# Performance work log

Hardware: AMD Instinct MI355X
Metric: run time of the kernel (lower is better)

## Reference

```python
import jax, jax.numpy as jnp
import numpy as np


def setup_inputs() -> dict:
    key = jax.random.key(0)
    k1, k2 = jax.random.split(key)
    B, S, D = 4, 2048, 1024
    x = jax.random.normal(k1, (B, S, D), dtype=jnp.float32)
    # uniform initializer in keras is small; scale to keep softmax well-behaved
    kernel = jax.random.normal(k2, (3, D, D), dtype=jnp.float32) * 0.02
    return {"x": x, "kernel": kernel}


def reference(x, kernel):
    # x: [B, S, D], kernel: [3, D, D]
    D = x.shape[-1]
    q = jnp.einsum('bsd,de->bse', x, kernel[0])
    k = jnp.einsum('bsd,de->bse', x, kernel[1])
    v = jnp.einsum('bsd,de->bse', x, kernel[2])
    scores = jnp.einsum('bqe,bke->bqk', q, k) / jnp.sqrt(jnp.float32(D))
    attn = jax.nn.softmax(scores, axis=-1)
    return jnp.einsum('bqk,bke->bqe', attn, v)
```

## Files before the change

### kernel.cpp

```cpp
#include <hip/hip_runtime.h>
#include <hip/hip_cooperative_groups.h>
#include <hip/hip_bf16.h>
#include <cstdint>

namespace cg = cooperative_groups;

typedef __bf16 bf16x8 __attribute__((ext_vector_type(8)));
typedef float f32x4 __attribute__((ext_vector_type(4)));

struct SharedMem {
  unsigned short As[2][4096];
  unsigned short Bs[2][4096];
};

__device__ __forceinline__ unsigned short f2bf(float f) {
  union { float f; uint32_t u; } a; a.f = f;
  uint32_t r = a.u + 0x7fffu + ((a.u >> 16) & 1u);
  return (unsigned short)(r >> 16);
}
__device__ __forceinline__ void gload_lds16(const unsigned short* g, unsigned short* l) {
  __builtin_amdgcn_global_load_lds(
      (const __attribute__((address_space(1))) void*)g,
      (__attribute__((address_space(3))) void*)l, 16, 0, 0);
}

template <int NJ>
__device__ __forceinline__ void gemm_tile_core(
    const unsigned short* __restrict__ A, const unsigned short* __restrict__ Bt,
    int K, SharedMem& sh, f32x4 (&acc)[4][NJ]) {
  const int t = threadIdx.x;
  const int lane = t & 63;
  const int quad = lane >> 4;
  const int l15 = lane & 15;
  const int wave = t >> 6;
  const int wm = (wave >> 1) * 64;
  const int wn = (wave & 1) * (NJ * 16);

  const int srow = t >> 2;
  const int scol = (((t & 3) ^ ((srow >> 1) & 3)) * 8);
  const unsigned short* ga = A + (size_t)srow * K + scol;
  const unsigned short* gb = Bt + (size_t)srow * K + scol;
  const size_t rowskip = (size_t)64 * K;

  const int swz = (quad ^ ((l15 >> 1) & 3)) * 8;
  const int aOff = (wm + l15) * 32 + swz;
  const int bOff = (wn + l15) * 32 + swz;

#pragma unroll
  for (int i = 0; i < 4; i++)
#pragma unroll
    for (int j = 0; j < NJ; j++) acc[i][j] = (f32x4){0.f, 0.f, 0.f, 0.f};

  gload_lds16(ga, &sh.As[0][t * 8]);
  gload_lds16(ga + rowskip, &sh.As[0][2048 + t * 8]);
  gload_lds16(gb, &sh.Bs[0][t * 8]);
  if (NJ == 4) gload_lds16(gb + rowskip, &sh.Bs[0][2048 + t * 8]);

  int buf = 0;
  for (int k0 = 0; k0 < K; k0 += 32, buf ^= 1) {
    __syncthreads();
    if (k0 + 32 < K) {
      const int kn = k0 + 32;
      gload_lds16(ga + kn, &sh.As[buf ^ 1][t * 8]);
      gload_lds16(ga + rowskip + kn, &sh.As[buf ^ 1][2048 + t * 8]);
      gload_lds16(gb + kn, &sh.Bs[buf ^ 1][t * 8]);
      if (NJ == 4) gload_lds16(gb + rowskip + kn, &sh.Bs[buf ^ 1][2048 + t * 8]);
    }
    const unsigned short* aB = &sh.As[buf][aOff];
    const unsigned short* bB = &sh.Bs[buf][bOff];
    bf16x8 a[4], b[NJ];
#pragma unroll
    for (int i = 0; i < 4; i++) a[i] = *(const bf16x8*)(aB + i * 512);
#pragma unroll
    for (int j = 0; j < NJ; j++) b[j] = *(const bf16x8*)(bB + j * 512);
#pragma unroll
    for (int i = 0; i < 4; i++)
#pragma unroll
      for (int j = 0; j < NJ; j++)
        acc[i][j] = __builtin_amdgcn_mfma_f32_16x16x32_bf16(a[i], b[j], acc[i][j], 0, 0, 0);
  }
}


__device__ __forceinline__ void phase0_casts(const float* __restrict__ x,
                                             const float* __restrict__ W,
                                             unsigned short* __restrict__ xb,
                                             unsigned short* __restrict__ Wt,
                                             SharedMem& sh) {
  const int bid = blockIdx.x, t = threadIdx.x;
#pragma unroll
  for (int i = 0; i < 4; i++) {
    size_t idx = (((size_t)(bid + i * 1024)) * 256 + t) * 8;
    float4 a = *(const float4*)(x + idx);
    float4 b = *(const float4*)(x + idx + 4);
    uint4 o;
    o.x = (uint32_t)f2bf(a.x) | ((uint32_t)f2bf(a.y) << 16);
    o.y = (uint32_t)f2bf(a.z) | ((uint32_t)f2bf(a.w) << 16);
    o.z = (uint32_t)f2bf(b.x) | ((uint32_t)f2bf(b.y) << 16);
    o.w = (uint32_t)f2bf(b.z) | ((uint32_t)f2bf(b.w) << 16);
    *(uint4*)(xb + idx) = o;
  }
  float* tile = (float*)sh.As;
  const int tx = t & 31, ty = t >> 5;
  for (int i = 0; i < 3; i++) {
    const int u = bid + i * 1024;
    const int z = u >> 10, rest = u & 1023;
    const float* Wz = W + (size_t)z * 1048576;
    unsigned short* Wtz = Wt + (size_t)z * 1048576;
    const int x0 = (rest & 31) * 32, y0 = (rest >> 5) * 32;
#pragma unroll
    for (int ii = 0; ii < 32; ii += 8)
      tile[(ty + ii) * 33 + tx] = Wz[(size_t)(y0 + ty + ii) * 1024 + x0 + tx];
    __syncthreads();
#pragma unroll
    for (int ii = 0; ii < 32; ii += 8)
      Wtz[(size_t)(x0 + ty + ii) * 1024 + y0 + tx] = f2bf(tile[tx * 33 + ty + ii]);
    __syncthreads();
  }
}

__device__ __forceinline__ void phase1_qkv(const unsigned short* __restrict__ xb,
                                           const unsigned short* __restrict__ Wt,
                                           unsigned short* __restrict__ Q,
                                           unsigned short* __restrict__ Kb,
                                           unsigned short* __restrict__ Vt,
                                           SharedMem& sh) {
  const int t = threadIdx.x;
  const int lane = t & 63, quad = lane >> 4, l15 = lane & 15, wave = t >> 6;
  const int wm = (wave >> 1) * 64;
  for (int pass = 0; pass < 2; pass++) {
    const int v = blockIdx.x + pass * 1024;
    if (v >= 1536) break;
    const int z = v >> 9, mt = (v >> 3) & 63, nt = v & 7;
    const unsigned short* A = xb + (size_t)mt * 128 * 1024;
    const unsigned short* Bt = Wt + (size_t)z * 1048576 + (size_t)nt * 128 * 1024;
    f32x4 acc[4][4];
    gemm_tile_core<4>(A, Bt, 1024, sh, acc);
    const int mbase = mt * 128 + wm + quad * 4;
    const int nbase = nt * 128 + (wave & 1) * 64 + l15;
    if (z < 2) {
      unsigned short* C = (z == 0) ? Q : Kb;
#pragma unroll
      for (int mi = 0; mi < 4; mi++)
#pragma unroll
        for (int ni = 0; ni < 4; ni++) {
          const int m = mbase + mi * 16, n = nbase + ni * 16;
#pragma unroll
          for (int r = 0; r < 4; r++)
            C[(size_t)(m + r) * 1024 + n] = f2bf(acc[mi][ni][r]);
        }
    } else {
#pragma unroll
      for (int mi = 0; mi < 4; mi++) {
        const int m = mbase + mi * 16;
        const int b = m >> 11, s = m & 2047;
#pragma unroll
        for (int ni = 0; ni < 4; ni++) {
          const int n = nbase + ni * 16;
          uint2 val;
          val.x = (uint32_t)f2bf(acc[mi][ni][0]) | ((uint32_t)f2bf(acc[mi][ni][1]) << 16);
          val.y = (uint32_t)f2bf(acc[mi][ni][2]) | ((uint32_t)f2bf(acc[mi][ni][3]) << 16);
          *(uint2*)(Vt + (size_t)b * 2097152 + (size_t)n * 2048 + s) = val;
        }
      }
    }
  }
}

__device__ __forceinline__ void phase2_scores(const unsigned short* __restrict__ Q,
                                              const unsigned short* __restrict__ Kb,
                                              unsigned short* __restrict__ Sb,
                                              float* __restrict__ partial,
                                              SharedMem& sh) {
  const int t = threadIdx.x;
  const int lane = t & 63, quad = lane >> 4, l15 = lane & 15, wave = t >> 6;
  const int wm = (wave >> 1) * 64;
  const int v = blockIdx.x;
  const int z = v >> 8, mt = (v >> 4) & 15, nt = v & 15;
  const unsigned short* A = Q + (size_t)z * 2097152 + (size_t)mt * 128 * 1024;
  const unsigned short* Bt = Kb + (size_t)z * 2097152 + (size_t)nt * 128 * 1024;
  f32x4 acc[4][4];
  gemm_tile_core<4>(A, Bt, 1024, sh, acc);
  unsigned short* C = Sb + (size_t)z * 4194304;
  const int mbase = mt * 128 + wm + quad * 4;
  const int nbase = nt * 128 + (wave & 1) * 64 + l15;
  const int j = nt * 2 + (wave & 1);
#pragma unroll
  for (int mi = 0; mi < 4; mi++) {
#pragma unroll
    for (int r = 0; r < 4; r++) {
      const int m = mbase + mi * 16 + r;
      float s = 0.f;
#pragma unroll
      for (int ni = 0; ni < 4; ni++) {
        const float e = __expf(acc[mi][ni][r] * 0.03125f);
        C[(size_t)m * 2048 + nbase + ni * 16] = f2bf(e);
        s += e;
      }
      s += __shfl_xor(s, 1);
      s += __shfl_xor(s, 2);
      s += __shfl_xor(s, 4);
      s += __shfl_xor(s, 8);
      if (l15 == 0) partial[(size_t)j * 8192 + (size_t)z * 2048 + m] = s;
    }
  }
}

__device__ __forceinline__ void phase3_pv(const unsigned short* __restrict__ Sb,
                                          const unsigned short* __restrict__ Vt,
                                          const float* __restrict__ partial,
                                          float* __restrict__ out,
                                          SharedMem& sh) {
  const int t = threadIdx.x;
  const int lane = t & 63, quad = lane >> 4, l15 = lane & 15, wave = t >> 6;
  const int wm = (wave >> 1) * 64;
  const int v = blockIdx.x;
  const int z = v >> 8, mt = (v >> 4) & 15, et = v & 15;
  const unsigned short* A = Sb + (size_t)z * 4194304 + (size_t)mt * 128 * 2048;
  const unsigned short* Bt = Vt + (size_t)z * 2097152 + (size_t)et * 64 * 2048;
  f32x4 acc[4][2];
  gemm_tile_core<2>(A, Bt, 2048, sh, acc);
  __syncthreads();
  float* rowinv = (float*)sh.As;
  if (t < 128) {
    const size_t grow = (size_t)z * 2048 + mt * 128 + t;
    float s = 0.f;
#pragma unroll 8
    for (int j = 0; j < 32; j++) s += partial[(size_t)j * 8192 + grow];
    rowinv[t] = 1.f / s;
  }
  __syncthreads();
  float* C = out + (size_t)z * 2097152;
  const int mbase = mt * 128 + wm + quad * 4;
  const int nbase = et * 64 + (wave & 1) * 32 + l15;
#pragma unroll
  for (int mi = 0; mi < 4; mi++) {
#pragma unroll
    for (int r = 0; r < 4; r++) {
      const int m = mbase + mi * 16 + r;
      const float inv = rowinv[m & 127];
#pragma unroll
      for (int ni = 0; ni < 2; ni++)
        C[(size_t)m * 1024 + nbase + ni * 16] = acc[mi][ni][r] * inv;
    }
  }
}

__global__ void __launch_bounds__(256, 4)
fused_attn(const float* __restrict__ x, const float* __restrict__ W,
           float* __restrict__ out, char* __restrict__ ws) {
  __shared__ SharedMem sh;
  unsigned short* xb = (unsigned short*)(ws);
  unsigned short* Wt = (unsigned short*)(ws + (16ll << 20));
  float* partial     = (float*)(ws + (16ll << 20));
  unsigned short* Q  = (unsigned short*)(ws + (22ll << 20));
  unsigned short* Kb = (unsigned short*)(ws + (38ll << 20));
  unsigned short* Vt = (unsigned short*)(ws + (54ll << 20));
  unsigned short* Sb = (unsigned short*)(ws + (70ll << 20));
  cg::grid_group grid = cg::this_grid();

  phase0_casts(x, W, xb, Wt, sh);
  grid.sync();
  phase1_qkv(xb, Wt, Q, Kb, Vt, sh);
  grid.sync();
  phase2_scores(Q, Kb, Sb, partial, sh);
  grid.sync();
  phase3_pv(Sb, Vt, partial, out, sh);
}

template <int P>
__global__ void __launch_bounds__(256)
phase_kernel(const float* __restrict__ x, const float* __restrict__ W,
             float* __restrict__ out, char* __restrict__ ws) {
  __shared__ SharedMem sh;
  unsigned short* xb = (unsigned short*)(ws);
  unsigned short* Wt = (unsigned short*)(ws + (16ll << 20));
  float* partial     = (float*)(ws + (16ll << 20));
  unsigned short* Q  = (unsigned short*)(ws + (22ll << 20));
  unsigned short* Kb = (unsigned short*)(ws + (38ll << 20));
  unsigned short* Vt = (unsigned short*)(ws + (54ll << 20));
  unsigned short* Sb = (unsigned short*)(ws + (70ll << 20));
  if (P == 0) phase0_casts(x, W, xb, Wt, sh);
  else if (P == 1) phase1_qkv(xb, Wt, Q, Kb, Vt, sh);
  else if (P == 2) phase2_scores(Q, Kb, Sb, partial, sh);
  else phase3_pv(Sb, Vt, partial, out, sh);
}

extern "C" void kernel_launch(void* const* d_in, const int* in_sizes, int n_in,
                              void* d_out, int out_size, void* d_ws, size_t ws_size,
                              hipStream_t stream) {
  const float* x = (const float*)d_in[0];
  const float* W = (const float*)d_in[1];
  float* out = (float*)d_out;
  char* ws = (char*)d_ws;

  int nb = 0;
  bool coop =
      (hipOccupancyMaxActiveBlocksPerMultiprocessor(&nb, (const void*)fused_attn, 256, 0) ==
       hipSuccess) && nb >= 4;
  if (coop) {
    void* args[] = {(void*)&x, (void*)&W, (void*)&out, (void*)&ws};
    coop = (hipLaunchCooperativeKernel((void*)fused_attn, dim3(1024), dim3(256), args, 0,
                                       stream) == hipSuccess);
  }
  if (!coop) {
    phase_kernel<0><<<1024, 256, 0, stream>>>(x, W, out, ws);
    phase_kernel<1><<<1024, 256, 0, stream>>>(x, W, out, ws);
    phase_kernel<2><<<1024, 256, 0, stream>>>(x, W, out, ws);
    phase_kernel<3><<<1024, 256, 0, stream>>>(x, W, out, ws);
  }
}
```

Before: 291.1 us.

## Replace cooperative grid-sync kernel with four separate phase launches

Removes the cooperative persistent kernel that used grid.sync between phases and always launches four separate phase kernels instead. Kernel boundaries now provide the cross-phase ordering, which avoids grid barrier cost and lets each phase drop the launch_bounds(256,4) occupancy constraint. It also adds a __syncthreads between passes in one phase, likely fixing an LDS reuse race. The cost is extra launch overhead and the loss of any cache locality carried between phases.

```diff
diff --git a/kernel.cpp b/kernel.cpp
--- a/kernel.cpp
+++ b/kernel.cpp
@@ -1,9 +1,6 @@
 #include <hip/hip_runtime.h>
-#include <hip/hip_cooperative_groups.h>
 #include <hip/hip_bf16.h>
 #include <cstdint>
-
-namespace cg = cooperative_groups;
 
 typedef __bf16 bf16x8 __attribute__((ext_vector_type(8)));
 typedef float f32x4 __attribute__((ext_vector_type(4)));
@@ -164,6 +161,7 @@
         }
       }
     }
+    if (pass == 0) __syncthreads();
   }
 }
 
@@ -244,28 +242,6 @@
         C[(size_t)m * 1024 + nbase + ni * 16] = acc[mi][ni][r] * inv;
     }
   }
-}
-
-__global__ void __launch_bounds__(256, 4)
-fused_attn(const float* __restrict__ x, const float* __restrict__ W,
-           float* __restrict__ out, char* __restrict__ ws) {
-  __shared__ SharedMem sh;
-  unsigned short* xb = (unsigned short*)(ws);
-  unsigned short* Wt = (unsigned short*)(ws + (16ll << 20));
-  float* partial     = (float*)(ws + (16ll << 20));
-  unsigned short* Q  = (unsigned short*)(ws + (22ll << 20));
-  unsigned short* Kb = (unsigned short*)(ws + (38ll << 20));
-  unsigned short* Vt = (unsigned short*)(ws + (54ll << 20));
-  unsigned short* Sb = (unsigned short*)(ws + (70ll << 20));
-  cg::grid_group grid = cg::this_grid();
-
-  phase0_casts(x, W, xb, Wt, sh);
-  grid.sync();
-  phase1_qkv(xb, Wt, Q, Kb, Vt, sh);
-  grid.sync();
-  phase2_scores(Q, Kb, Sb, partial, sh);
-  grid.sync();
-  phase3_pv(Sb, Vt, partial, out, sh);
 }
 
 template <int P>
@@ -293,20 +269,8 @@
   const float* W = (const float*)d_in[1];
   float* out = (float*)d_out;
   char* ws = (char*)d_ws;
-
-  int nb = 0;
-  bool coop =
-      (hipOccupancyMaxActiveBlocksPerMultiprocessor(&nb, (const void*)fused_attn, 256, 0) ==
-       hipSuccess) && nb >= 4;
-  if (coop) {
-    void* args[] = {(void*)&x, (void*)&W, (void*)&out, (void*)&ws};
-    coop = (hipLaunchCooperativeKernel((void*)fused_attn, dim3(1024), dim3(256), args, 0,
-                                       stream) == hipSuccess);
-  }
-  if (!coop) {
-    phase_kernel<0><<<1024, 256, 0, stream>>>(x, W, out, ws);
-    phase_kernel<1><<<1024, 256, 0, stream>>>(x, W, out, ws);
-    phase_kernel<2><<<1024, 256, 0, stream>>>(x, W, out, ws);
-    phase_kernel<3><<<1024, 256, 0, stream>>>(x, W, out, ws);
-  }
-}
+  phase_kernel<0><<<1024, 256, 0, stream>>>(x, W, out, ws);
+  phase_kernel<1><<<1024, 256, 0, stream>>>(x, W, out, ws);
+  phase_kernel<2><<<1024, 256, 0, stream>>>(x, W, out, ws);
+  phase_kernel<3><<<1024, 256, 0, stream>>>(x, W, out, ws);
+}
```

Measured after the change: 290.5 us. No clear change (-0.2%).
